# Performance work log

Hardware: AMD Instinct MI355X
Metric: run time of the kernel (lower is better)

Reference implementation:

```python
import jax, jax.numpy as jnp
import numpy as np

THRESHOLD = 0.3

def setup_inputs() -> dict:
    key = jax.random.key(0)
    ks = jax.random.split(key, 8)
    B, T, N, d = 4, 32, 1024, 2
    hd, od, hs, osz = 64, 64, 128, 2
    p = lambda k, sh: jax.random.normal(k, sh, jnp.float32) * 0.1
    return {
        "points": jax.random.uniform(ks[0], (B, T, N, d), jnp.float32),
        "W1": p(ks[1], (hd, d)),   "b1": jnp.zeros((hd,), jnp.float32),
        "W2": p(ks[2], (od, hd)),  "b2": jnp.zeros((od,), jnp.float32),
        "Wg": p(ks[3], (hd, od)),  "bg": jnp.zeros((hd,), jnp.float32),
        "Wih": p(ks[4], (3 * hs, hd)), "Whh": p(ks[5], (3 * hs, hs)),
        "bih": jnp.zeros((3 * hs,), jnp.float32), "bhh": jnp.zeros((3 * hs,), jnp.float32),
        "Wf": p(ks[6], (osz, hs)), "bf": jnp.zeros((osz,), jnp.float32),
    }

def _gcn_step(pts, W1, b1, W2, b2, Wg, bg):
    # pts: [N, d]. Torch detaches node features & adjacency (no grad to points).
    pts = jax.lax.stop_gradient(pts)
    dist = jnp.linalg.norm(pts[:, None, :] - pts[None, :, :], axis=2)  # [N,N]
    A = (dist < THRESHOLD).astype(pts.dtype)
    dinv = 1.0 / jnp.sqrt(A.sum(axis=1))          # rowsum >= 1 (self-loop)
    An = A * dinv[:, None] * dinv[None, :]        # D^{-1/2} A D^{-1/2}
    x = jax.nn.relu((An @ pts) @ W1.T + b1)       # [N, hd]
    x = jax.nn.relu((An @ x) @ W2.T + b2)         # [N, od]
    return x.mean(axis=0) @ Wg.T + bg             # [hd]

def reference(points, W1, b1, W2, b2, Wg, bg, Wih, Whh, bih, bhh, Wf, bf):
    # GCN per (batch, time): [B, T, hd]
    gcn = jax.vmap(jax.vmap(lambda p: _gcn_step(p, W1, b1, W2, b2, Wg, bg)))(points)
    H = Whh.shape[1]

    def gru_step(h, x):  # torch GRU gate order: r, z, n
        gi = x @ Wih.T + bih
        gh = h @ Whh.T + bhh
        ir, iz, inn = jnp.split(gi, 3)
        hr, hz, hn = jnp.split(gh, 3)
        r = jax.nn.sigmoid(ir + hr)
        z = jax.nn.sigmoid(iz + hz)
        n = jnp.tanh(inn + r * hn)
        h_new = (1.0 - z) * n + z * h
        return h_new, h_new

    h0 = jnp.zeros((H,), points.dtype)
    run = lambda xs: jax.lax.scan(gru_step, h0, xs)[1]   # [T, H]
    hs = jax.vmap(run)(gcn)                              # [B, T, H]
    y = hs @ Wf.T + bf                                   # [B, T, out]
    # torch: per-element gru_out.mean(dim=1, keepdim=True) on [1,T,out] -> [1,1,out], stacked -> [B,1,1,out]
    return y.mean(axis=1, keepdims=True)[:, :, None, :]
```

## Files before the change

### kernel.cpp

```cpp
#include <hip/hip_runtime.h>
#include <hip/hip_bf16.h>
#include <math.h>

#define N_PTS 1024
#define BT    128
typedef unsigned int u32;
typedef __attribute__((ext_vector_type(8))) short short8_t;
typedef __attribute__((ext_vector_type(4))) float f32x4;
typedef __fp16 fp16x2 __attribute__((ext_vector_type(2)));
typedef _Float16 f16x2 __attribute__((ext_vector_type(2)));

#if defined(__has_builtin)
#if __has_builtin(__builtin_amdgcn_fdot2)
#define HAVE_FDOT2 1
#endif
#endif
#ifndef HAVE_FDOT2
#define HAVE_FDOT2 0
#endif

__device__ __forceinline__ float bfi(u32 bits16) {
    union { u32 u; float f; } v; v.u = bits16 << 16; return v.f;
}
__device__ __forceinline__ unsigned short f2bf(float f) {
    union { float f; u32 u; } v; v.f = f;
    return (unsigned short)((v.u + 0x7FFFu + ((v.u >> 16) & 1u)) >> 16);
}
__device__ __forceinline__ u32 pkbf(float a, float b) {
    union { __hip_bfloat162 b2; u32 u; } cv;
    cv.b2 = __float22bfloat162_rn(make_float2(a, b));
    return cv.u;
}
__device__ __forceinline__ u32 pkh(float a, float b) {
    union { fp16x2 h; u32 u; } c; c.h = __builtin_amdgcn_cvt_pkrtz(a, b); return c.u;
}
__device__ __forceinline__ unsigned short f16b(float v) {
    union { fp16x2 h; unsigned short s[2]; } c;
    c.h = __builtin_amdgcn_cvt_pkrtz(v, 0.0f);
    return c.s[0];
}
#if HAVE_FDOT2
__device__ __forceinline__ float fdot2h(u32 a, u32 b, float c) {
    union { u32 u; f16x2 h; } A, B; A.u = a; B.u = b;
    return __builtin_amdgcn_fdot2(A.h, B.h, c, false);
}
#else
__device__ __forceinline__ float fdot2h(u32 a, u32 b, float c) {
    union { u32 u; _Float16 h[2]; } A, B; A.u = a; B.u = b;
    return fmaf((float)A.h[0], (float)B.h[0], fmaf((float)A.h[1], (float)B.h[1], c));
}
#endif
__device__ __forceinline__ float ldf(const void* p, int i, bool bf) {
    return bf ? bfi(((const unsigned short*)p)[i]) : ((const float*)p)[i];
}
__device__ __forceinline__ float2 ldp(const void* pbase, int j, bool bf) {
    if (bf) {
        u32 w = ((const u32*)pbase)[j];
        return make_float2(bfi(w & 0xFFFFu), bfi(w >> 16));
    }
    return ((const float2*)pbase)[j];
}
__device__ __forceinline__ bool detect_bf16(const void* pts, int tid, int* s_flag) {
    if (tid < 64) {
        u32 w = ((const u32*)pts)[tid];
        float v = bfi(w & 0xFFFFu);
        bool ok = (v >= 0.0f) && (v <= 1.0f);
        unsigned long long m = __ballot(ok);
        if (tid == 0) *s_flag = (m == 0xFFFFFFFFFFFFFFFFull) ? 1 : 0;
    }
    __syncthreads();
    return *s_flag != 0;
}
__device__ __forceinline__ bool is_nb(float px, float py, float qx, float qy) {
    float dx = px - qx, dy = py - qy;
    float d2 = __fadd_rn(__fmul_rn(dx, dx), __fmul_rn(dy, dy));
    return d2 < 0.09f;
}
__device__ __forceinline__ const void* pts_base(const void* pts, int bt, bool bf) {
    return bf ? (const void*)((const unsigned short*)pts + (size_t)bt * N_PTS * 2)
              : (const void*)((const float*)pts + (size_t)bt * N_PTS * 2);
}
__device__ __forceinline__ void gload16(const u32* g, u32* l) {
    __builtin_amdgcn_global_load_lds((const __attribute__((address_space(1))) u32*)g,
                                     (__attribute__((address_space(3))) u32*)l, 16, 0, 0);
}
__device__ __forceinline__ u32 rdlaneu(u32 v, int i) {
    return (u32)__builtin_amdgcn_readlane((int)v, i);
}
__device__ __forceinline__ float sigm(float x) {
    return __fdividef(1.0f, 1.0f + __expf(-x));
}
__device__ __forceinline__ float tanh_f(float x) {
    return fmaf(2.0f, __fdividef(1.0f, 1.0f + __expf(-2.0f * x)), -1.0f);
}

__global__ __launch_bounds__(256) void k1_bm(const void* __restrict__ pts,
                                             float* __restrict__ dinv,
                                             float* __restrict__ gsum,
                                             u32* __restrict__ bm) {
    int blk = blockIdx.x, tid = threadIdx.x;
    int bt = blk >> 2, q = blk & 3;
    __shared__ float2 sp[N_PTS];
    __shared__ int s_flag;
    bool bf = detect_bf16(pts, tid, &s_flag);
    const void* pb = pts_base(pts, bt, bf);
    for (int j = tid; j < N_PTS; j += 256) sp[j] = ldp(pb, j, bf);
    if (blk < 32) gsum[blk * 256 + tid] = 0.0f;
    __syncthreads();
    int i = q * 256 + tid;
    float px = sp[i].x, py = sp[i].y;
    const float4* sp4 = (const float4*)sp;
    u32* bmrow = bm + (size_t)bt * 32768 + i;
    int cnt = 0;
    for (int c = 0; c < 32; c++) {
        u32 m = 0;
#pragma unroll
        for (int h = 0; h < 8; h++) {
            float4 s01 = sp4[c * 16 + 2 * h], s23 = sp4[c * 16 + 2 * h + 1];
            if (is_nb(px, py, s01.x, s01.y)) m |= 1u << (4 * h);
            if (is_nb(px, py, s01.z, s01.w)) m |= 1u << (4 * h + 1);
            if (is_nb(px, py, s23.x, s23.y)) m |= 1u << (4 * h + 2);
            if (is_nb(px, py, s23.z, s23.w)) m |= 1u << (4 * h + 3);
        }
        bmrow[c * 1024] = m;
        cnt += __popc(m);
    }
    dinv[bt * N_PTS + i] = 1.0f / sqrtf((float)cnt);
}

__global__ __launch_bounds__(256) void k3a_x1v(const void* __restrict__ pts,
                                               const void* __restrict__ W1,
                                               const void* __restrict__ b1,
                                               const float* __restrict__ dinv,
                                               const u32* __restrict__ bm,
                                               u32* __restrict__ x1vB) {
    __shared__ u32 pool[10944];
    __shared__ int s_flag;
    float* poolf = (float*)pool;
    float2* sud = (float2*)pool;
    u32* bmL = pool + 2048;
    float* sdiL = poolf + 10496;
    float* b1L = poolf + 10752;
    float* W1L = poolf + 10816;
    int tid = threadIdx.x, lane = tid & 63, w = tid >> 6;
    int l15 = lane & 15, quad = lane >> 4;
    int blk = blockIdx.x, bt = blk & 127, rowblk = blk >> 7;
    int rowbase = rowblk * 256;
    bool bf = detect_bf16(pts, tid, &s_flag);
    const void* pb = pts_base(pts, bt, bf);
    for (int j = tid; j < N_PTS; j += 256) {
        float2 p = ldp(pb, j, bf);
        float d = dinv[bt * N_PTS + j];
        sud[j] = make_float2(d * p.x, d * p.y);
    }
    sdiL[tid] = dinv[bt * N_PTS + rowbase + tid];
    for (int idx = tid; idx < 8192; idx += 256) {
        int c = idx >> 8, r = idx & 255;
        bmL[r * 33 + c] = bm[(size_t)bt * 32768 + c * 1024 + rowbase + r];
    }
    if (tid < 128) W1L[tid] = ldf(W1, tid, bf);
    if (tid < 64)  b1L[tid] = ldf(b1, tid, bf);
    __syncthreads();

    float w0v[4], w1v[4], b1v[4];
#pragma unroll
    for (int nb = 0; nb < 4; nb++) {
        int ch = nb * 16 + l15;
        w0v[nb] = W1L[2 * ch]; w1v[nb] = W1L[2 * ch + 1]; b1v[nb] = b1L[ch];
    }
    f32x4 acc[4][4];
#pragma unroll
    for (int rf = 0; rf < 4; rf++)
#pragma unroll
        for (int nb = 0; nb < 4; nb++)
#pragma unroll
            for (int r = 0; r < 4; r++) acc[rf][nb][r] = 0.0f;

    for (int ks = 0; ks < 32; ks++) {
        const float4* u4 = (const float4*)(sud + ks * 32 + quad * 8);
        float4 U0 = u4[0], U1 = u4[1], U2 = u4[2], U3 = u4[3];
        float pxd[8] = {U0.x, U0.z, U1.x, U1.z, U2.x, U2.z, U3.x, U3.z};
        float pyd[8] = {U0.y, U0.w, U1.y, U1.w, U2.y, U2.w, U3.y, U3.w};
        short8_t bz[4];
#pragma unroll
        for (int nb = 0; nb < 4; nb++) {
            union { short8_t v; u32 d[4]; } cv;
#pragma unroll
            for (int p = 0; p < 4; p++) {
                float z0 = fmaf(pxd[2 * p],     w0v[nb], pyd[2 * p]     * w1v[nb]);
                float z1 = fmaf(pxd[2 * p + 1], w0v[nb], pyd[2 * p + 1] * w1v[nb]);
                cv.d[p] = pkbf(z0, z1);
            }
            bz[nb] = cv.v;
        }
#pragma unroll
        for (int rf = 0; rf < 4; rf++) {
            u32 word = bmL[(w * 64 + rf * 16 + l15) * 33 + ks];
            u32 by = (word >> (quad * 8)) & 0xFFu;
            short8_t av;
#pragma unroll
            for (int i2 = 0; i2 < 8; i2++)
                av[i2] = (by & (1u << i2)) ? (short)0x3F80 : (short)0;
#pragma unroll
            for (int nb = 0; nb < 4; nb++)
                acc[rf][nb] = __builtin_amdgcn_mfma_f32_16x16x32_bf16(av, bz[nb], acc[rf][nb], 0, 0, 0);
        }
    }
    __syncthreads();
    u32* dumpX = pool + 2048;
#pragma unroll
    for (int rf = 0; rf < 4; rf++) {
        float4 dv = *(const float4*)(sdiL + w * 64 + rf * 16 + quad * 4);
        float dva[4] = {dv.x, dv.y, dv.z, dv.w};
#pragma unroll
        for (int nb = 0; nb < 4; nb++) {
            int ch = nb * 16 + l15;
            float xo[4];
#pragma unroll
            for (int r = 0; r < 4; r++) {
                float tq = fmaf(dva[r], acc[rf][nb][r], b1v[nb]);
                xo[r] = dva[r] * fmaxf(tq, 0.0f);
            }
            u32 dbase = (u32)(ch * 132 + w * 32 + rf * 8 + quad * 2);
            *(uint2*)(dumpX + dbase) = make_uint2(pkbf(xo[0], xo[1]), pkbf(xo[2], xo[3]));
        }
    }
    __syncthreads();
    int ch = tid >> 2, seg = tid & 3;
    u32* gbase = x1vB + ((size_t)(bt * 16 + rowblk * 4) * 64) * 36;
#pragma unroll
    for (int t4 = 0; t4 < 4; t4++) {
        const uint4* src = (const uint4*)(dumpX + ch * 132 + t4 * 32 + seg * 8);
        uint4 v0 = src[0], v1 = src[1];
        u32* dst = gbase + ((size_t)(t4 * 64 + ch)) * 36 + seg * 8;
        *(uint4*)dst = v0; *(uint4*)(dst + 4) = v1;
    }
}

__global__ __launch_bounds__(256) void k3_mfma(const void* __restrict__ pts,
                                               const void* __restrict__ W2,
                                               const void* __restrict__ b2,
                                               const float* __restrict__ dinv,
                                               const u32* __restrict__ bm,
                                               const u32* __restrict__ x1vB,
                                               float* __restrict__ gsum) {
    __shared__ u32 pool[15424];
    __shared__ int s_flag;
    float* poolf = (float*)pool;
    int tid = threadIdx.x, lane = tid & 63, w = tid >> 6;
    int l15 = lane & 15, quad = lane >> 4;
    int blk = blockIdx.x, bt = blk & 127, rowblk = blk >> 7;
    bool bf = detect_bf16(pts, tid, &s_flag);

    const u32* xg = x1vB + (size_t)bt * 36864;
    for (int it = w; it < 9; it += 4)
        gload16(xg + it * 256 + lane * 4, pool + 8192 + it * 256 + lane * 4);

    const u32* bg_ = bm + (size_t)bt * 32768 + rowblk * 256;
    for (int idx = tid; idx < 8192; idx += 256) {
        int c = idx >> 8, r = idx & 255;
        pool[idx] = bg_[c * 1024 + r];
    }
    unsigned short* W2B = (unsigned short*)(pool + 12800);
    for (int idx = tid; idx < 4096; idx += 256) {
        int o = idx >> 6, c = idx & 63;
        W2B[o * 72 + c] = f2bf(ldf(W2, idx, bf));
    }
    if (tid < 256) poolf[15104 + tid] = dinv[bt * N_PTS + rowblk * 256 + tid];
    if (tid < 64)  poolf[15360 + tid] = ldf(b2, tid, bf);

    f32x4 acc[4][4];
#pragma unroll
    for (int rf = 0; rf < 4; rf++)
#pragma unroll
        for (int nb = 0; nb < 4; nb++)
#pragma unroll
            for (int r = 0; r < 4; r++) acc[rf][nb][r] = 0.0f;

    for (int t = 0; t < 16; t++) {
        __syncthreads();
        if (t + 1 < 16) {
            u32* dst = pool + ((t & 1) ? 8192 : 10496);
            const u32* src = xg + (t + 1) * 2304;
            for (int it = w; it < 9; it += 4)
                gload16(src + it * 256 + lane * 4, dst + it * 256 + lane * 4);
        }
        const unsigned short* xf = (const unsigned short*)(pool + ((t & 1) ? 10496 : 8192));
#pragma unroll
        for (int ks = 0; ks < 2; ks++) {
            short8_t bq[4];
#pragma unroll
            for (int rf = 0; rf < 4; rf++) {
                u32 mw = pool[(2 * t + ks) * 256 + w * 64 + rf * 16 + l15];
                u32 by = (mw >> (quad * 8)) & 0xFFu;
                short8_t v;
#pragma unroll
                for (int i2 = 0; i2 < 8; i2++)
                    v[i2] = (by & (1u << i2)) ? (short)0x3F80 : (short)0;
                bq[rf] = v;
            }
#pragma unroll
            for (int nb = 0; nb < 4; nb++) {
                short8_t af = *(const short8_t*)(xf + (nb * 16 + l15) * 72 + ks * 32 + quad * 8);
#pragma unroll
                for (int rf = 0; rf < 4; rf++)
                    acc[rf][nb] = __builtin_amdgcn_mfma_f32_16x16x32_bf16(af, bq[rf], acc[rf][nb], 0, 0, 0);
            }
        }
    }
    __syncthreads();

    u32* dump = pool;
#pragma unroll
    for (int rf = 0; rf < 4; rf++) {
        int rn = w * 64 + rf * 16 + l15;
        float di = poolf[15104 + rn];
#pragma unroll
        for (int nb = 0; nb < 4; nb++) {
            u32 lo = (u32)f2bf(acc[rf][nb][0] * di) | ((u32)f2bf(acc[rf][nb][1] * di) << 16);
            u32 hi = (u32)f2bf(acc[rf][nb][2] * di) | ((u32)f2bf(acc[rf][nb][3] * di) << 16);
            u32* dst = dump + rn * 36 + nb * 8 + quad * 2;
            dst[0] = lo; dst[1] = hi;
        }
    }
    __syncthreads();
    f32x4 xacc[4][4];
#pragma unroll
    for (int ob = 0; ob < 4; ob++)
#pragma unroll
        for (int rf = 0; rf < 4; rf++)
#pragma unroll
            for (int r = 0; r < 4; r++) xacc[ob][rf][r] = 0.0f;
#pragma unroll
    for (int ks2 = 0; ks2 < 2; ks2++) {
        short8_t b2f[4];
#pragma unroll
        for (int rf = 0; rf < 4; rf++)
            b2f[rf] = *(const short8_t*)((const unsigned short*)dump +
                        (w * 64 + rf * 16 + l15) * 72 + ks2 * 32 + quad * 8);
#pragma unroll
        for (int ob = 0; ob < 4; ob++) {
            short8_t a2 = *(const short8_t*)(W2B + (ob * 16 + l15) * 72 + ks2 * 32 + quad * 8);
#pragma unroll
            for (int rf = 0; rf < 4; rf++)
                xacc[ob][rf] = __builtin_amdgcn_mfma_f32_16x16x32_bf16(a2, b2f[rf], xacc[ob][rf], 0, 0, 0);
        }
    }
#pragma unroll
    for (int ob = 0; ob < 4; ob++) {
#pragma unroll
        for (int r = 0; r < 4; r++) {
            int o = ob * 16 + quad * 4 + r;
            float bb = poolf[15360 + o];
            float s = 0.0f;
#pragma unroll
            for (int rf = 0; rf < 4; rf++) s += fmaxf(xacc[ob][rf][r] + bb, 0.0f);
            s += __shfl_down(s, 8, 16);
            s += __shfl_down(s, 4, 16);
            s += __shfl_down(s, 2, 16);
            s += __shfl_down(s, 1, 16);
            if (l15 == 0) atomicAdd(&gsum[bt * 64 + o], s);
        }
    }
}

__global__ __launch_bounds__(768, 1) void k4_all(const void* __restrict__ pts,
                                                 const void* __restrict__ Wg,
                                                 const void* __restrict__ bg,
                                                 const void* __restrict__ Wih,
                                                 const void* __restrict__ Whh,
                                                 const void* __restrict__ bih,
                                                 const void* __restrict__ bhh,
                                                 const void* __restrict__ Wf,
                                                 const void* __restrict__ bf_,
                                                 const float* __restrict__ gsum,
                                                 float* __restrict__ out) {
    int b = blockIdx.x, tid = threadIdx.x;
    __shared__ float s_gir[4096];
    __shared__ float s_giz[4096];
    __shared__ float s_gin[4096];
    __shared__ float sWgT[64 * 65];
    __shared__ float s_gm[2048];
    __shared__ float s_x[2048];
    __shared__ float s_pt[768];
    __shared__ unsigned short s_hp[128];
    __shared__ int s_flag;
    bool bf = detect_bf16(pts, tid, &s_flag);
    int lane = tid & 63, wv = tid >> 6;
    int l15 = lane & 15, quad = lane >> 4;
    int hi = (tid >= 384) ? 1 : 0;
    int r = tid - hi * 384;

    for (int idx = tid; idx < 4096; idx += 768) {
        int o = idx >> 6, k = idx & 63;
        sWgT[k * 65 + o] = ldf(Wg, idx, bf);
    }
    for (int idx = tid; idx < 2048; idx += 768)
        s_gm[idx] = gsum[(size_t)b * 2048 + idx] * (1.0f / 1024.0f);
    __syncthreads();
    for (int idx = tid; idx < 2048; idx += 768) {
        int t = idx >> 6, c = idx & 63;
        float s0 = ldf(bg, c, bf), s1 = 0.f, s2 = 0.f, s3 = 0.f;
        const float* gm = s_gm + t * 64;
#pragma unroll
        for (int k = 0; k < 64; k += 4) {
            s0 = fmaf(sWgT[k * 65 + c],       gm[k],     s0);
            s1 = fmaf(sWgT[(k + 1) * 65 + c], gm[k + 1], s1);
            s2 = fmaf(sWgT[(k + 2) * 65 + c], gm[k + 2], s2);
            s3 = fmaf(sWgT[(k + 3) * 65 + c], gm[k + 3], s3);
        }
        s_x[idx] = (s0 + s1) + (s2 + s3);
    }
    u32 whp[32];
    {
        int koff = r * 128 + hi * 64;
        if (bf) {
            const u32* wp = (const u32*)Whh + koff / 2;
#pragma unroll
            for (int m = 0; m < 32; m++) {
                u32 wq = wp[m];
                whp[m] = pkh(bfi(wq & 0xFFFFu), bfi(wq >> 16));
            }
        } else {
            const float2* wp = (const float2*)Whh + koff / 2;
#pragma unroll
            for (int m = 0; m < 32; m++) {
                float2 v = wp[m];
                whp[m] = pkh(v.x, v.y);
            }
        }
    }
    float bhr = hi ? 0.0f : ldf(bhh, r, bf);
    __syncthreads();

    {
        short8_t Ah[2][2], Al[2][2];
#pragma unroll
        for (int mt = 0; mt < 2; mt++)
#pragma unroll
            for (int ks = 0; ks < 2; ks++) {
                const float* xs = s_x + (mt * 16 + l15) * 64 + ks * 32 + quad * 8;
                short8_t ah, al;
#pragma unroll
                for (int i = 0; i < 8; i++) {
                    float v = xs[i];
                    unsigned short hb = f2bf(v);
                    ah[i] = (short)hb;
                    al[i] = (short)f2bf(v - bfi(hb));
                }
                Ah[mt][ks] = ah; Al[mt][ks] = al;
            }
#pragma unroll
        for (int ni = 0; ni < 2; ni++) {
            int nt = wv * 2 + ni;
            int c = nt * 16 + l15;
            float bv = ldf(bih, c, bf);
            short8_t Bh[2], Bl[2];
#pragma unroll
            for (int ks = 0; ks < 2; ks++) {
                int base = c * 64 + ks * 32 + quad * 8;
                short8_t bh, bl;
#pragma unroll
                for (int i = 0; i < 8; i++) {
                    float v = ldf(Wih, base + i, bf);
                    unsigned short hb = f2bf(v);
                    bh[i] = (short)hb;
                    bl[i] = (short)f2bf(v - bfi(hb));
                }
                Bh[ks] = bh; Bl[ks] = bl;
            }
            float* gdst = ((nt >> 3) == 0) ? s_gir : (((nt >> 3) == 1) ? s_giz : s_gin);
            int cpart = (nt & 7) * 16 + l15;
#pragma unroll
            for (int mt = 0; mt < 2; mt++) {
                f32x4 acc; acc[0] = bv; acc[1] = bv; acc[2] = bv; acc[3] = bv;
#pragma unroll
                for (int ks = 0; ks < 2; ks++) {
                    acc = __builtin_amdgcn_mfma_f32_16x16x32_bf16(Ah[mt][ks], Bh[ks], acc, 0, 0, 0);
                    acc = __builtin_amdgcn_mfma_f32_16x16x32_bf16(Ah[mt][ks], Bl[ks], acc, 0, 0, 0);
                    acc = __builtin_amdgcn_mfma_f32_16x16x32_bf16(Al[mt][ks], Bh[ks], acc, 0, 0, 0);
                }
#pragma unroll
                for (int rr2 = 0; rr2 < 4; rr2++) {
                    int t = mt * 16 + quad * 4 + rr2;
                    gdst[t * 128 + cpart] = acc[rr2];
                }
            }
        }
    }
    int slot = (r >> 7) * 2 + hi;
    int cpart = r & 127;
    float h_self = 0.0f, hsum = 0.0f;
    u32 hpreg = 0;
    __syncthreads();

    for (int t = 0; t < 32; t++) {
        float s0 = bhr, s1 = 0.f, s2 = 0.f, s3 = 0.f;
#pragma unroll
        for (int m = 0; m < 32; m += 4) {
            s0 = fdot2h(whp[m],     rdlaneu(hpreg, m),     s0);
            s1 = fdot2h(whp[m + 1], rdlaneu(hpreg, m + 1), s1);
            s2 = fdot2h(whp[m + 2], rdlaneu(hpreg, m + 2), s2);
            s3 = fdot2h(whp[m + 3], rdlaneu(hpreg, m + 3), s3);
        }
        s_pt[slot * 128 + cpart] = (s0 + s1) + (s2 + s3);
        __syncthreads();
        if (tid < 128) {
            int c = tid;
            float gr = s_gir[t * 128 + c] + s_pt[c]       + s_pt[128 + c];
            float gz = s_giz[t * 128 + c] + s_pt[256 + c] + s_pt[384 + c];
            float hn = s_pt[512 + c] + s_pt[640 + c];
            float rr = sigm(gr);
            float zz = sigm(gz);
            float n  = tanh_f(fmaf(rr, hn, s_gin[t * 128 + c]));
            float hnew = fmaf(zz, h_self - n, n);
            h_self = hnew; hsum += hnew;
            s_hp[c] = f16b(hnew);
        }
        __syncthreads();
        hpreg = ((const u32*)s_hp)[hi * 32 + (lane & 31)];
    }
    if (tid < 128) s_gm[tid] = hsum;
    __syncthreads();
    if (tid < 128) {
        float hm = s_gm[tid] * (1.0f / 32.0f);
        s_gm[256 + tid] = ldf(Wf, tid, bf) * hm;
        s_gm[384 + tid] = ldf(Wf, 128 + tid, bf) * hm;
    }
    __syncthreads();
    if (tid < 2) {
        float s = ldf(bf_, tid, bf);
        for (int k = 0; k < 128; k++) s += s_gm[256 + tid * 128 + k];
        out[b * 2 + tid] = s;
    }
}

extern "C" void kernel_launch(void* const* d_in, const int* in_sizes, int n_in,
                              void* d_out, int out_size, void* d_ws, size_t ws_size,
                              hipStream_t stream) {
    const void* pts = d_in[0];
    const void* W1  = d_in[1];
    const void* b1  = d_in[2];
    const void* W2  = d_in[3];
    const void* b2  = d_in[4];
    const void* Wg  = d_in[5];
    const void* bg  = d_in[6];
    const void* Wih = d_in[7];
    const void* Whh = d_in[8];
    const void* bih = d_in[9];
    const void* bhh = d_in[10];
    const void* Wf  = d_in[11];
    const void* bf_ = d_in[12];

    float* dinv = (float*)d_ws;
    float* gsum = dinv + (size_t)BT * N_PTS;
    u32*   bm   = (u32*)(gsum + BT * 64);
    u32*   x1vB = bm + (size_t)BT * 32768;

    k1_bm  <<<512, 256, 0, stream>>>(pts, dinv, gsum, bm);
    k3a_x1v<<<512, 256, 0, stream>>>(pts, W1, b1, dinv, bm, x1vB);
    k3_mfma<<<512, 256, 0, stream>>>(pts, W2, b2, dinv, bm, x1vB, gsum);
    k4_all <<<4, 768, 0, stream>>>(pts, Wg, bg, Wih, Whh, bih, bhh, Wf, bf_,
                                   gsum, (float*)d_out);
}
```

Before: 240.8 us.

## Fuse three GCN kernels into one cooperative kernel with grid syncs

Merges the adjacency-bitmask, first-layer and MFMA second-layer kernels into one cooperative launch, using grid-wide syncs between phases instead of separate kernel launches. A non-cooperative three-launch fallback is kept. This removes inter-kernel launch gaps, at the cost of a shared, larger LDS allocation for all phases, a 2-blocks-per-CU launch bound that may limit registers, and grid barrier overhead.

```diff
diff --git a/kernel.cpp b/kernel.cpp
--- a/kernel.cpp
+++ b/kernel.cpp
@@ -1,6 +1,9 @@
 #include <hip/hip_runtime.h>
 #include <hip/hip_bf16.h>
+#include <hip/hip_cooperative_groups.h>
 #include <math.h>
+
+namespace cg = cooperative_groups;
 
 #define N_PTS 1024
 #define BT    128
@@ -94,15 +97,11 @@
     return fmaf(2.0f, __fdividef(1.0f, 1.0f + __expf(-2.0f * x)), -1.0f);
 }
 
-__global__ __launch_bounds__(256) void k1_bm(const void* __restrict__ pts,
-                                             float* __restrict__ dinv,
-                                             float* __restrict__ gsum,
-                                             u32* __restrict__ bm) {
-    int blk = blockIdx.x, tid = threadIdx.x;
+__device__ void phase1_body(const void* __restrict__ pts, float* __restrict__ dinv,
+                            float* __restrict__ gsum, u32* __restrict__ bm,
+                            u32* pool, bool bf, int blk, int tid) {
+    float2* sp = (float2*)pool;
     int bt = blk >> 2, q = blk & 3;
-    __shared__ float2 sp[N_PTS];
-    __shared__ int s_flag;
-    bool bf = detect_bf16(pts, tid, &s_flag);
     const void* pb = pts_base(pts, bt, bf);
     for (int j = tid; j < N_PTS; j += 256) sp[j] = ldp(pb, j, bf);
     if (blk < 32) gsum[blk * 256 + tid] = 0.0f;
@@ -128,25 +127,20 @@
     dinv[bt * N_PTS + i] = 1.0f / sqrtf((float)cnt);
 }
 
-__global__ __launch_bounds__(256) void k3a_x1v(const void* __restrict__ pts,
-                                               const void* __restrict__ W1,
-                                               const void* __restrict__ b1,
-                                               const float* __restrict__ dinv,
-                                               const u32* __restrict__ bm,
-                                               u32* __restrict__ x1vB) {
-    __shared__ u32 pool[10944];
-    __shared__ int s_flag;
+__device__ void phase2_body(const void* __restrict__ pts, const void* __restrict__ W1,
+                            const void* __restrict__ b1, const float* __restrict__ dinv,
+                            const u32* __restrict__ bm, u32* __restrict__ x1vB,
+                            u32* pool, bool bf, int blk, int tid) {
     float* poolf = (float*)pool;
     float2* sud = (float2*)pool;
     u32* bmL = pool + 2048;
     float* sdiL = poolf + 10496;
     float* b1L = poolf + 10752;
     float* W1L = poolf + 10816;
-    int tid = threadIdx.x, lane = tid & 63, w = tid >> 6;
+    int lane = tid & 63, w = tid >> 6;
     int l15 = lane & 15, quad = lane >> 4;
-    int blk = blockIdx.x, bt = blk & 127, rowblk = blk >> 7;
+    int bt = blk & 127, rowblk = blk >> 7;
     int rowbase = rowblk * 256;
-    bool bf = detect_bf16(pts, tid, &s_flag);
     const void* pb = pts_base(pts, bt, bf);
     for (int j = tid; j < N_PTS; j += 256) {
         float2 p = ldp(pb, j, bf);
@@ -237,20 +231,14 @@
     }
 }
 
-__global__ __launch_bounds__(256) void k3_mfma(const void* __restrict__ pts,
-                                               const void* __restrict__ W2,
-                                               const void* __restrict__ b2,
-                                               const float* __restrict__ dinv,
-                                               const u32* __restrict__ bm,
-                                               const u32* __restrict__ x1vB,
-                                               float* __restrict__ gsum) {
-    __shared__ u32 pool[15424];
-    __shared__ int s_flag;
+__device__ void phase3_body(const void* __restrict__ W2, const void* __restrict__ b2,
+                            const float* __restrict__ dinv, const u32* __restrict__ bm,
+                            const u32* __restrict__ x1vB, float* __restrict__ gsum,
+                            u32* pool, bool bf, int blk, int tid) {
     float* poolf = (float*)pool;
-    int tid = threadIdx.x, lane = tid & 63, w = tid >> 6;
+    int lane = tid & 63, w = tid >> 6;
     int l15 = lane & 15, quad = lane >> 4;
-    int blk = blockIdx.x, bt = blk & 127, rowblk = blk >> 7;
-    bool bf = detect_bf16(pts, tid, &s_flag);
+    int bt = blk & 127, rowblk = blk >> 7;
 
     const u32* xg = x1vB + (size_t)bt * 36864;
     for (int it = w; it < 9; it += 4)
@@ -362,6 +350,32 @@
             if (l15 == 0) atomicAdd(&gsum[bt * 64 + o], s);
         }
     }
+}
+
+__global__ __launch_bounds__(256, 2) void coop_pipe(const void* __restrict__ pts,
+                                                    const void* __restrict__ W1,
+                                                    const void* __restrict__ b1,
+                                                    const void* __restrict__ W2,
+                                                    const void* __restrict__ b2,
+                                                    float* __restrict__ dinv,
+                                                    float* __restrict__ gsum,
+                                                    u32* __restrict__ bm,
+                                                    u32* __restrict__ x1vB,
+                                                    int phase) {
+    __shared__ u32 pool[15424];
+    __shared__ int s_flag;
+    int tid = threadIdx.x, blk = blockIdx.x;
+    bool bf = detect_bf16(pts, tid, &s_flag);
+    cg::grid_group grid = cg::this_grid();
+
+    if (phase <= 1)
+        phase1_body(pts, dinv, gsum, bm, pool, bf, blk, tid);
+    if (phase == 0) { __threadfence(); grid.sync(); __syncthreads(); }
+    if (phase == 0 || phase == 2)
+        phase2_body(pts, W1, b1, dinv, bm, x1vB, pool, bf, blk, tid);
+    if (phase == 0) { __threadfence(); grid.sync(); __syncthreads(); }
+    if (phase == 0 || phase == 3)
+        phase3_body(W2, b2, dinv, bm, x1vB, gsum, pool, bf, blk, tid);
 }
 
 __global__ __launch_bounds__(768, 1) void k4_all(const void* __restrict__ pts,
@@ -557,9 +571,17 @@
     u32*   bm   = (u32*)(gsum + BT * 64);
     u32*   x1vB = bm + (size_t)BT * 32768;
 
-    k1_bm  <<<512, 256, 0, stream>>>(pts, dinv, gsum, bm);
-    k3a_x1v<<<512, 256, 0, stream>>>(pts, W1, b1, dinv, bm, x1vB);
-    k3_mfma<<<512, 256, 0, stream>>>(pts, W2, b2, dinv, bm, x1vB, gsum);
-    k4_all <<<4, 768, 0, stream>>>(pts, Wg, bg, Wih, Whh, bih, bhh, Wf, bf_,
-                                   gsum, (float*)d_out);
-}
+    int phase0 = 0;
+    void* cargs[] = { (void*)&pts, (void*)&W1, (void*)&b1, (void*)&W2, (void*)&b2,
+                      (void*)&dinv, (void*)&gsum, (void*)&bm, (void*)&x1vB,
+                      (void*)&phase0 };
+    hipError_t ce = hipLaunchCooperativeKernel((const void*)coop_pipe,
+                                               dim3(512), dim3(256), cargs, 0, stream);
+    if (ce != hipSuccess) {
+        coop_pipe<<<512, 256, 0, stream>>>(pts, W1, b1, W2, b2, dinv, gsum, bm, x1vB, 1);
+        coop_pipe<<<512, 256, 0, stream>>>(pts, W1, b1, W2, b2, dinv, gsum, bm, x1vB, 2);
+        coop_pipe<<<512, 256, 0, stream>>>(pts, W1, b1, W2, b2, dinv, gsum, bm, x1vB, 3);
+    }
+    k4_all<<<4, 768, 0, stream>>>(pts, Wg, bg, Wih, Whh, bih, bhh, Wf, bf_,
+                                  gsum, (float*)d_out);
+}
```

Result: slower. 453.8 us (+88.5%).
